# Performance work log

Measured on AMD Instinct MI355X. Metric: run time of the kernel, lower is better.

## Reference

```python
import jax, jax.numpy as jnp
import numpy as np

K = 2
NUM_EXPERTS = 8
NOISE_EPS = 1e-2
GATE_EPS = 1e-6
LOG_EPS = float(np.finfo(np.float64).eps)


def _cv_squared(x):
    # torch .var() is unbiased (ddof=1)
    x = x.astype(jnp.float32)
    return jnp.var(x, ddof=1) / (jnp.mean(x) ** 2 + 1e-10)


def _normal_cdf(x):
    return 0.5 * (1.0 + jax.lax.erf(x * np.float32(1.0 / np.sqrt(2.0))))


def _noisy_top_k_gating(x, noise, w_gate, w_noise):
    B = x.shape[0]
    clean_logits = x @ w_gate                                   # [B, E]
    noise_stddev = jax.nn.softplus(x @ w_noise) + NOISE_EPS     # [B, E]
    noisy_logits = clean_logits + noise * noise_stddev
    probs = jax.nn.softmax(noisy_logits, axis=1)                # softmax before top-k (as in source)
    m = min(K + 1, NUM_EXPERTS)
    top_p, top_idx = jax.lax.top_k(probs, m)                    # [B, m]
    top_k_p = top_p[:, :K]
    top_k_idx = top_idx[:, :K]
    top_k_gates = top_k_p / (jnp.sum(top_k_p, axis=1, keepdims=True) + GATE_EPS)
    gates = jnp.zeros_like(probs).at[jnp.arange(B)[:, None], top_k_idx].set(top_k_gates)
    # load via prob-in-top-k (noisy branch, k < num_experts)
    thr_in = top_p[:, K][:, None]        # (k+1)-th top value
    thr_out = top_p[:, K - 1][:, None]   # k-th top value
    is_in = noisy_logits > thr_in
    prob_if_in = _normal_cdf((clean_logits - thr_in) / noise_stddev)
    prob_if_out = _normal_cdf((clean_logits - thr_out) / noise_stddev)
    load = jnp.sum(jnp.where(is_in, prob_if_in, prob_if_out), axis=0)  # [E]
    return gates, load


def _expert_combine(feat, W, gates):
    # feat [B, D], W [E, D, C], gates [B, E]; expert = linear head + log_softmax
    log_p = jax.nn.log_softmax(jnp.einsum('bd,edc->bec', feat, W), axis=-1)  # [B, E, C]
    # combine: exp(log-scores) * gate, scatter-add over batch, clamp zeros, log
    combined = jnp.einsum('be,bec->bc', gates, jnp.exp(log_p))
    combined = jnp.where(combined == 0, LOG_EPS, combined)
    return jnp.log(combined)


def _moe_forward(sf, of, ppf, pvf, noise, w_gate, w_noise, Ws, Wo, Wp):
    gates, load = _noisy_top_k_gating(sf, noise, w_gate, w_noise)
    importance = jnp.sum(gates, axis=0)
    loss = (_cv_squared(importance) + _cv_squared(load)) * 1e-2
    pf = jnp.concatenate([ppf, pvf], axis=1)  # predicate head input
    ys = _expert_combine(sf, Ws, gates)
    yo = _expert_combine(of, Wo, gates)
    yp = _expert_combine(pf, Wp, gates)
    return ys, yo, yp, loss


def setup_inputs() -> dict:
    key = jax.random.key(0)
    ks = jax.random.split(key, 10)
    B, D, DP, E, C = 4096, 1024, 512, NUM_EXPERTS, 256
    inv = np.float32(1.0 / np.sqrt(D))
    return {
        'sf': jax.random.normal(ks[0], (B, D), jnp.float32),
        'of': jax.random.normal(ks[1], (B, D), jnp.float32),
        'ppf': jax.random.normal(ks[2], (B, DP), jnp.float32),
        'pvf': jax.random.normal(ks[3], (B, DP), jnp.float32),
        'noise': jax.random.normal(ks[4], (B, E), jnp.float32),
        'w_gate': jax.random.normal(ks[5], (D, E), jnp.float32) * 0.02,
        'w_noise': jax.random.normal(ks[6], (D, E), jnp.float32) * 0.02,
        'Ws': jax.random.normal(ks[7], (E, D, C), jnp.float32) * inv,
        'Wo': jax.random.normal(ks[8], (E, D, C), jnp.float32) * inv,
        'Wp': jax.random.normal(ks[9], (E, 2 * DP, C), jnp.float32) * inv,
    }


def reference(sf, of, ppf, pvf, noise, w_gate, w_noise, Ws, Wo, Wp):
    return _moe_forward(sf, of, ppf, pvf, noise, w_gate, w_noise, Ws, Wo, Wp)
```

## Files before the change

### kernel.cpp

```cpp
#include <hip/hip_runtime.h>
#include <math.h>

#define NB 4096
#define DD 1024
#define CC 256
#define NE 8
#define NGBLK 1024

typedef short bf16x8 __attribute__((ext_vector_type(8)));
typedef float f32x4 __attribute__((ext_vector_type(4)));

#define WT_OFF   262144ull
#define PART_OFF 13631488ull
#define PART_ROWS 8224
#define WS_FAST_NEED (41943040ull)

__device__ __forceinline__ unsigned short f2bf(float f) {
    union { float f; unsigned u; } v; v.f = f;
    unsigned x = v.u;
    return (unsigned short)((x + 0x7FFFu + ((x >> 16) & 1u)) >> 16);
}

__global__ __launch_bounds__(256) void gating_kernel(
    const float* __restrict__ sf, const float* __restrict__ noise,
    const float* __restrict__ wg, const float* __restrict__ wn,
    float* __restrict__ gval, int* __restrict__ eidx,
    float* __restrict__ cnt_p, float* __restrict__ imp_p, float* __restrict__ load_p)
{
    int t = threadIdx.x;
    int lane = t & 63;
    int w = t >> 6;
    int b = blockIdx.x * 4 + w;
    const float* x = sf + (size_t)b * DD;

    float accg[8], accn[8];
#pragma unroll
    for (int e = 0; e < 8; e++) { accg[e] = 0.f; accn[e] = 0.f; }

#pragma unroll
    for (int q = 0; q < 16; q++) {
        int d = q * 64 + lane;
        float xs = x[d];
        float4 g0 = *(const float4*)(wg + (size_t)d * 8);
        float4 g1 = *(const float4*)(wg + (size_t)d * 8 + 4);
        float4 n0 = *(const float4*)(wn + (size_t)d * 8);
        float4 n1 = *(const float4*)(wn + (size_t)d * 8 + 4);
        accg[0] += xs * g0.x; accg[1] += xs * g0.y; accg[2] += xs * g0.z; accg[3] += xs * g0.w;
        accg[4] += xs * g1.x; accg[5] += xs * g1.y; accg[6] += xs * g1.z; accg[7] += xs * g1.w;
        accn[0] += xs * n0.x; accn[1] += xs * n0.y; accn[2] += xs * n0.z; accn[3] += xs * n0.w;
        accn[4] += xs * n1.x; accn[5] += xs * n1.y; accn[6] += xs * n1.z; accn[7] += xs * n1.w;
    }
#pragma unroll
    for (int e = 0; e < 8; e++) {
        for (int s = 1; s < 64; s <<= 1) {
            accg[e] += __shfl_xor(accg[e], s);
            accn[e] += __shfl_xor(accn[e], s);
        }
    }

    __shared__ float s_load[4][8], s_imp[4][8], s_cnt[4][8];

    if (lane == 0) {
        float clean[8], stdv[8], noisy[8], p[8];
        float mx = -1e30f;
#pragma unroll
        for (int e = 0; e < 8; e++) {
            clean[e] = accg[e];
            float xn = accn[e];
            float sp = (xn > 0.f) ? (xn + log1pf(expf(-xn))) : log1pf(expf(xn));
            stdv[e] = sp + 0.01f;
            noisy[e] = clean[e] + noise[(size_t)b * 8 + e] * stdv[e];
            mx = fmaxf(mx, noisy[e]);
        }
        float se = 0.f;
#pragma unroll
        for (int e = 0; e < 8; e++) { p[e] = expf(noisy[e] - mx); se += p[e]; }
        float inv = 1.f / se;
#pragma unroll
        for (int e = 0; e < 8; e++) p[e] *= inv;

        int i0 = -1, i1 = -1;
        float p0 = -1e30f, p1v = -1e30f, p2v = -1e30f;
#pragma unroll
        for (int e = 0; e < 8; e++) if (p[e] > p0) { p0 = p[e]; i0 = e; }
#pragma unroll
        for (int e = 0; e < 8; e++) if (e != i0 && p[e] > p1v) { p1v = p[e]; i1 = e; }
#pragma unroll
        for (int e = 0; e < 8; e++) if (e != i0 && e != i1 && p[e] > p2v) { p2v = p[e]; }

        float den = p0 + p1v + 1e-6f;
        float g0 = p0 / den, g1 = p1v / den;
        eidx[2 * b] = i0; eidx[2 * b + 1] = i1;
        gval[2 * b] = g0; gval[2 * b + 1] = g1;

        const float is2 = 0.70710678118654752440f;
#pragma unroll
        for (int e = 0; e < 8; e++) {
            float pin  = 0.5f * (1.f + erff((clean[e] - p2v) / stdv[e] * is2));
            float pout = 0.5f * (1.f + erff((clean[e] - p1v) / stdv[e] * is2));
            s_load[w][e] = (noisy[e] > p2v) ? pin : pout;
            s_imp[w][e]  = (e == i0) ? g0 : (e == i1) ? g1 : 0.f;
            s_cnt[w][e]  = (e == i0 || e == i1) ? 1.f : 0.f;
        }
    }
    __syncthreads();
    if (t < 8) {
        float sl = 0.f, si = 0.f, sc = 0.f;
#pragma unroll
        for (int ww = 0; ww < 4; ww++) {
            sl += s_load[ww][t]; si += s_imp[ww][t]; sc += s_cnt[ww][t];
        }
        load_p[blockIdx.x * 8 + t] = sl;
        imp_p [blockIdx.x * 8 + t] = si;
        cnt_p [blockIdx.x * 8 + t] = sc;
    }
}

__global__ void scan_loss_kernel(const float* __restrict__ cnt_p, const float* __restrict__ imp_p,
                                 const float* __restrict__ load_p,
                                 int* __restrict__ counts, int* __restrict__ off,
                                 int* __restrict__ toff32, int* __restrict__ toff64,
                                 float* __restrict__ out_loss)
{
    __shared__ float s_c[64], s_i[64], s_l[64];
    __shared__ float f_c[8], f_i[8], f_l[8];
    int t = threadIdx.x;
    int e = t & 7, g = t >> 3;
    float sc = 0.f, si = 0.f, sl = 0.f;
    for (int blk = g * 128; blk < (g + 1) * 128; blk++) {
        sc += cnt_p[blk * 8 + e];
        si += imp_p[blk * 8 + e];
        sl += load_p[blk * 8 + e];
    }
    s_c[t] = sc; s_i[t] = si; s_l[t] = sl;
    __syncthreads();
    if (t < 8) {
        float c = 0.f, i = 0.f, l = 0.f;
        for (int gg = 0; gg < 8; gg++) { c += s_c[gg * 8 + t]; i += s_i[gg * 8 + t]; l += s_l[gg * 8 + t]; }
        f_c[t] = c; f_i[t] = i; f_l[t] = l;
        counts[t] = (int)(c + 0.5f);
    }
    __syncthreads();
    if (t == 0) {
        int o = 0, t32 = 0, t64 = 0;
        off[0] = 0; toff32[0] = 0; toff64[0] = 0;
        for (int ee = 0; ee < 8; ee++) {
            int c = (int)(f_c[ee] + 0.5f);
            o += c; off[ee + 1] = o;
            t32 += (c + 31) / 32; toff32[ee + 1] = t32;
            t64 += (c + 63) / 64; toff64[ee + 1] = t64;
        }
        float mi = 0.f, ml = 0.f;
        for (int ee = 0; ee < 8; ee++) { mi += f_i[ee]; ml += f_l[ee]; }
        mi *= 0.125f; ml *= 0.125f;
        float vi = 0.f, vl = 0.f;
        for (int ee = 0; ee < 8; ee++) {
            float di = f_i[ee] - mi; vi += di * di;
            float dl = f_l[ee] - ml; vl += dl * dl;
        }
        vi /= 7.f; vl /= 7.f;
        out_loss[0] = (vi / (mi * mi + 1e-10f) + vl / (ml * ml + 1e-10f)) * 0.01f;
    }
}

__global__ __launch_bounds__(256) void fill_kernel(
    const int* __restrict__ eidx, const int* __restrict__ off, int* __restrict__ rowlist)
{
    __shared__ int hist[256][8];
    __shared__ int off_s[8];
    int t = threadIdx.x;
    if (t < 8) off_s[t] = off[t];
    int base = t * 32;
    int le[32];
    int c[8];
#pragma unroll
    for (int e = 0; e < 8; e++) c[e] = 0;
#pragma unroll
    for (int j = 0; j < 32; j++) {
        int ev = eidx[base + j];
        le[j] = ev;
#pragma unroll
        for (int e = 0; e < 8; e++) c[e] += (ev == e) ? 1 : 0;
    }
#pragma unroll
    for (int e = 0; e < 8; e++) hist[t][e] = c[e];
    __syncthreads();
    if (t < 8) {
        int run = 0;
        for (int i = 0; i < 256; i++) { int v = hist[i][t]; hist[i][t] = run; run += v; }
    }
    __syncthreads();
#pragma unroll
    for (int j = 0; j < 32; j++) {
        int ev = le[j];
        int p = hist[t][ev];
        hist[t][ev] = p + 1;
        rowlist[off_s[ev] + p] = base + j;
    }
}

__global__ __launch_bounds__(256) void prep_w_kernel(
    const float* __restrict__ Ws, const float* __restrict__ Wo, const float* __restrict__ Wp,
    unsigned short* __restrict__ Wt)
{
    __shared__ unsigned short LT[64][68];
    int bid = blockIdx.x;
    int ep = bid >> 6;
    int rem = bid & 63;
    int k0 = (rem >> 2) * 64;
    int c0 = (rem & 3) * 64;
    int strm = ep >> 3, e = ep & 7;
    const float* W = ((strm == 0) ? Ws : (strm == 1) ? Wo : Wp) + (size_t)e * (1024 * 256);

    int t = threadIdx.x;
    int c_l = t & 63;
    int kb = t >> 6;
#pragma unroll
    for (int r = 0; r < 16; r++) {
        int k_l = r * 4 + kb;
        LT[c_l][k_l] = f2bf(W[(size_t)(k0 + k_l) * 256 + c0 + c_l]);
    }
    __syncthreads();

    int cw = t >> 2, kq = t & 3;
    unsigned short* dst_row = Wt + (size_t)ep * 262144 + (size_t)(c0 + cw) * 1024 + k0;
#pragma unroll
    for (int p = 0; p < 2; p++) {
        int kqp = kq + p * 4;
        ushort4 a = *(ushort4*)&LT[cw][kqp * 8];
        ushort4 b = *(ushort4*)&LT[cw][kqp * 8 + 4];
        uint4 o;
        o.x = (unsigned)a.x | ((unsigned)a.y << 16);
        o.y = (unsigned)a.z | ((unsigned)a.w << 16);
        o.z = (unsigned)b.x | ((unsigned)b.y << 16);
        o.w = (unsigned)b.z | ((unsigned)b.w << 16);
        *(uint4*)(dst_row + kqp * 8) = o;
    }
}

__global__ __launch_bounds__(512) void combine_mfma_kernel(
    const float* __restrict__ sf, const float* __restrict__ of,
    const float* __restrict__ ppf, const float* __restrict__ pvf,
    const unsigned short* __restrict__ Wt,
    const int* __restrict__ counts, const int* __restrict__ off, const int* __restrict__ toff64,
    const int* __restrict__ rowlist, const float* __restrict__ gval,
    float* __restrict__ partial)
{
    int bid = blockIdx.x;
    int strm = blockIdx.z;
    if (bid >= toff64[8]) return;
    int e = 0;
    while (bid >= toff64[e + 1]) e++;
    int tm = bid - toff64[e];
    int cnt = counts[e];
    int obase = off[e];
    int ep = strm * 8 + e;

    __shared__ unsigned short A_lds[2][64 * 64];
    __shared__ unsigned short B_lds[2][256 * 64];

    int t = threadIdx.x;
    int l = t & 63, w = t >> 6;
    int wr = w >> 2, wc = w & 3;

    int sm = t >> 3;
    int ss = t & 7;
    int m_st = tm * 64 + sm;
    int pid_st = (m_st < cnt) ? rowlist[obase + m_st] : 8192;
    int arow = (pid_st >= 8192) ? 0 : (pid_st >> 1);
    const float* a01 = (strm == 0) ? (sf + (size_t)arow * DD) : (of + (size_t)arow * DD);
    const float* app = ppf + (size_t)arow * 512;
    const float* apv = pvf + (size_t)arow * 512;
    const unsigned short* bsrc = Wt + (size_t)ep * 262144 + (size_t)sm * 1024 + ss * 8;
    int aw = sm * 64 + ((ss ^ (sm & 7)) * 8);
    int bw = (ss ^ (sm & 7)) * 8;

#define LOAD_A(ko, dst)                                                    \
    {                                                                      \
        int kk = (ko) + ss * 8;                                            \
        const float* s_;                                                   \
        if (strm != 2) s_ = a01 + kk;                                      \
        else s_ = (kk < 512) ? (app + kk) : (apv + (kk - 512));            \
        float4 f0 = *(const float4*)s_;                                    \
        float4 f1 = *(const float4*)(s_ + 4);                              \
        dst.x = (unsigned)f2bf(f0.x) | ((unsigned)f2bf(f0.y) << 16);       \
        dst.y = (unsigned)f2bf(f0.z) | ((unsigned)f2bf(f0.w) << 16);       \
        dst.z = (unsigned)f2bf(f1.x) | ((unsigned)f2bf(f1.y) << 16);       \
        dst.w = (unsigned)f2bf(f1.z) | ((unsigned)f2bf(f1.w) << 16);       \
    }

    {
        uint4 ra; LOAD_A(0, ra);
        uint4 rb[4];
#pragma unroll
        for (int q = 0; q < 4; q++) rb[q] = *(const uint4*)(bsrc + q * 65536);
        *(uint4*)&A_lds[0][aw] = ra;
#pragma unroll
        for (int q = 0; q < 4; q++) *(uint4*)&B_lds[0][(sm + q * 64) * 64 + bw] = rb[q];
    }

    f32x4 acc[2][4];
#pragma unroll
    for (int i = 0; i < 2; i++)
#pragma unroll
        for (int j = 0; j < 4; j++)
#pragma unroll
            for (int r = 0; r < 4; r++) acc[i][j][r] = 0.f;

    int g = l >> 4;
    int axor = l & 7;

    for (int kt = 0; kt < 16; kt++) {
        int cur = kt & 1;
        uint4 ra; uint4 rb[4];
        if (kt < 15) {
            int ko = (kt + 1) * 64;
            LOAD_A(ko, ra);
#pragma unroll
            for (int q = 0; q < 4; q++) rb[q] = *(const uint4*)(bsrc + q * 65536 + ko);
        }
        __syncthreads();
#pragma unroll
        for (int kw = 0; kw < 2; kw++) {
            int slot = ((kw * 4 + g) ^ axor) * 8;
            bf16x8 af[2], bf[4];
#pragma unroll
            for (int i = 0; i < 2; i++)
                af[i] = *(const bf16x8*)&A_lds[cur][(wr * 32 + (l & 15) + i * 16) * 64 + slot];
#pragma unroll
            for (int j = 0; j < 4; j++)
                bf[j] = *(const bf16x8*)&B_lds[cur][(wc * 64 + j * 16 + (l & 15)) * 64 + slot];
#pragma unroll
            for (int i = 0; i < 2; i++)
#pragma unroll
                for (int j = 0; j < 4; j++)
                    acc[i][j] = __builtin_amdgcn_mfma_f32_16x16x32_bf16(af[i], bf[j], acc[i][j], 0, 0, 0);
        }
        if (kt < 15) {
            *(uint4*)&A_lds[cur ^ 1][aw] = ra;
#pragma unroll
            for (int q = 0; q < 4; q++) *(uint4*)&B_lds[cur ^ 1][(sm + q * 64) * 64 + bw] = rb[q];
        }
    }
#undef LOAD_A

    __syncthreads();
    float* s_red = (float*)&A_lds[0][0];

    float gate_r[2][4];
    int pid_r[2][4];
#pragma unroll
    for (int i = 0; i < 2; i++)
#pragma unroll
        for (int r = 0; r < 4; r++) {
            int row = wr * 32 + i * 16 + g * 4 + r;
            int m = tm * 64 + row;
            int pid = (m < cnt) ? rowlist[obase + m] : 8192;
            pid_r[i][r] = pid;
            gate_r[i][r] = (m < cnt) ? gval[pid] : 0.f;
        }

    float rmx[2][4], scale[2][4];
#pragma unroll
    for (int i = 0; i < 2; i++)
#pragma unroll
        for (int r = 0; r < 4; r++) {
            float mx = -1e30f;
#pragma unroll
            for (int j = 0; j < 4; j++) mx = fmaxf(mx, acc[i][j][r]);
#pragma unroll
            for (int s = 1; s < 16; s <<= 1) mx = fmaxf(mx, __shfl_xor(mx, s));
            if ((l & 15) == 0) s_red[(wr * 32 + i * 16 + g * 4 + r) * 4 + wc] = mx;
        }
    __syncthreads();
#pragma unroll
    for (int i = 0; i < 2; i++)
#pragma unroll
        for (int r = 0; r < 4; r++) {
            int row = wr * 32 + i * 16 + g * 4 + r;
            rmx[i][r] = fmaxf(fmaxf(s_red[row * 4 + 0], s_red[row * 4 + 1]),
                              fmaxf(s_red[row * 4 + 2], s_red[row * 4 + 3]));
        }
    __syncthreads();
#pragma unroll
    for (int i = 0; i < 2; i++)
#pragma unroll
        for (int r = 0; r < 4; r++) {
            float se = 0.f;
#pragma unroll
            for (int j = 0; j < 4; j++) {
                float v = __expf(acc[i][j][r] - rmx[i][r]);
                acc[i][j][r] = v;
                se += v;
            }
#pragma unroll
            for (int s = 1; s < 16; s <<= 1) se += __shfl_xor(se, s);
            if ((l & 15) == 0) s_red[(wr * 32 + i * 16 + g * 4 + r) * 4 + wc] = se;
        }
    __syncthreads();
#pragma unroll
    for (int i = 0; i < 2; i++)
#pragma unroll
        for (int r = 0; r < 4; r++) {
            int row = wr * 32 + i * 16 + g * 4 + r;
            float tot = s_red[row * 4 + 0] + s_red[row * 4 + 1] + s_red[row * 4 + 2] + s_red[row * 4 + 3];
            scale[i][r] = gate_r[i][r] / tot;
        }

    float* pbase = partial + (size_t)strm * (PART_ROWS * 256);
#pragma unroll
    for (int i = 0; i < 2; i++)
#pragma unroll
        for (int r = 0; r < 4; r++) {
            float* pr = pbase + (size_t)pid_r[i][r] * 256;
            float sc = scale[i][r];
#pragma unroll
            for (int j = 0; j < 4; j++) {
                int col = wc * 64 + j * 16 + (l & 15);
                pr[col] = acc[i][j][r] * sc;
            }
        }
}

__global__ void log_pair_kernel(const float* __restrict__ partial, float* __restrict__ out, int n4)
{
    int i = blockIdx.x * 256 + threadIdx.x;
    if (i >= n4) return;
    int flat = i * 4;
    int strm = flat >> 20;
    int rem = flat & 1048575;
    int b = rem >> 8;
    int c = rem & 255;
    const float* p0 = partial + (size_t)strm * (PART_ROWS * 256) + (size_t)(2 * b) * 256 + c;
    float4 v0 = *(const float4*)p0;
    float4 v1 = *(const float4*)(p0 + 256);
    const float EPSL = 2.2204460492503131e-16f;
    float4 v;
    v.x = v0.x + v1.x; v.y = v0.y + v1.y; v.z = v0.z + v1.z; v.w = v0.w + v1.w;
    v.x = logf(v.x == 0.f ? EPSL : v.x);
    v.y = logf(v.y == 0.f ? EPSL : v.y);
    v.z = logf(v.z == 0.f ? EPSL : v.z);
    v.w = logf(v.w == 0.f ? EPSL : v.w);
    *(float4*)(out + (size_t)flat) = v;
}

__global__ __launch_bounds__(256) void combine_kernel(
    const float* __restrict__ sf, const float* __restrict__ of,
    const float* __restrict__ ppf, const float* __restrict__ pvf,
    const float* __restrict__ Ws, const float* __restrict__ Wo, const float* __restrict__ Wp,
    const int* __restrict__ counts, const int* __restrict__ off, const int* __restrict__ toff,
    const int* __restrict__ rowlist, const float* __restrict__ gval,
    float* __restrict__ out)
{
    int bid = blockIdx.x;
    int strm = blockIdx.z;
    if (bid >= toff[8]) return;
    int e = 0;
    while (bid >= toff[e + 1]) e++;
    int tm = bid - toff[e];
    int cnt = counts[e];
    int obase = off[e];

    __shared__ float As[32][36];
    __shared__ float Bs[32][256];
    __shared__ int rows_s[32];
    __shared__ float gate_s[32];

    int t = threadIdx.x;
    if (t < 32) {
        int m = tm * 32 + t;
        if (m < cnt) {
            int pid = rowlist[obase + m];
            rows_s[t] = pid >> 1;
            gate_s[t] = gval[pid];
        } else {
            rows_s[t] = -1;
            gate_s[t] = 0.f;
        }
    }
    __syncthreads();

    const float* W = ((strm == 0) ? Ws : (strm == 1) ? Wo : Wp) + (size_t)e * DD * CC;
    float acc[2][16];
#pragma unroll
    for (int i = 0; i < 2; i++)
#pragma unroll
        for (int j = 0; j < 16; j++) acc[i][j] = 0.f;

    int tx = t & 15, ty = t >> 4;
    int r_st = t >> 3, d4 = t & 7;
    int row_st = rows_s[r_st];

    for (int k0 = 0; k0 < DD; k0 += 32) {
        float4 v = make_float4(0.f, 0.f, 0.f, 0.f);
        if (row_st >= 0) {
            int d = k0 + d4 * 4;
            if (strm == 0)      v = *(const float4*)(sf + (size_t)row_st * DD + d);
            else if (strm == 1) v = *(const float4*)(of + (size_t)row_st * DD + d);
            else v = (d < 512) ? *(const float4*)(ppf + (size_t)row_st * 512 + d)
                               : *(const float4*)(pvf + (size_t)row_st * 512 + (d - 512));
        }
        As[d4 * 4 + 0][r_st] = v.x;
        As[d4 * 4 + 1][r_st] = v.y;
        As[d4 * 4 + 2][r_st] = v.z;
        As[d4 * 4 + 3][r_st] = v.w;
#pragma unroll
        for (int j = 0; j < 8; j++) {
            int vv = t + 256 * j;
            int k = vv >> 6, c4 = vv & 63;
            *(float4*)&Bs[k][c4 * 4] = *(const float4*)&W[(size_t)(k0 + k) * CC + c4 * 4];
        }
        __syncthreads();

#pragma unroll
        for (int k = 0; k < 32; k++) {
            float2 a = *(float2*)&As[k][ty * 2];
#pragma unroll
            for (int jj = 0; jj < 4; jj++) {
                float4 bb = *(float4*)&Bs[k][jj * 64 + tx * 4];
                acc[0][jj * 4 + 0] += a.x * bb.x;
                acc[0][jj * 4 + 1] += a.x * bb.y;
                acc[0][jj * 4 + 2] += a.x * bb.z;
                acc[0][jj * 4 + 3] += a.x * bb.w;
                acc[1][jj * 4 + 0] += a.y * bb.x;
                acc[1][jj * 4 + 1] += a.y * bb.y;
                acc[1][jj * 4 + 2] += a.y * bb.z;
                acc[1][jj * 4 + 3] += a.y * bb.w;
            }
        }
        __syncthreads();
    }

    float* comb = out + (size_t)strm * (NB * CC);
#pragma unroll
    for (int i = 0; i < 2; i++) {
        int r = ty * 2 + i;
        int row = rows_s[r];
        if (row < 0) continue;
        float mx = -1e30f;
#pragma unroll
        for (int j = 0; j < 16; j++) mx = fmaxf(mx, acc[i][j]);
        for (int s = 1; s < 16; s <<= 1) mx = fmaxf(mx, __shfl_xor(mx, s, 16));
        float se = 0.f;
#pragma unroll
        for (int j = 0; j < 16; j++) { acc[i][j] = expf(acc[i][j] - mx); se += acc[i][j]; }
        for (int s = 1; s < 16; s <<= 1) se += __shfl_xor(se, s, 16);
        float scale = gate_s[r] / se;
#pragma unroll
        for (int jj = 0; jj < 4; jj++)
#pragma unroll
            for (int jo = 0; jo < 4; jo++) {
                int col = jj * 64 + tx * 4 + jo;
                atomicAdd(comb + (size_t)row * CC + col, acc[i][jj * 4 + jo] * scale);
            }
    }
}

__global__ void log_kernel(float* __restrict__ out, int n4)
{
    int i = blockIdx.x * 256 + threadIdx.x;
    if (i >= n4) return;
    float4 v = *(float4*)(out + (size_t)i * 4);
    const float EPSL = 2.2204460492503131e-16f;
    v.x = logf(v.x == 0.f ? EPSL : v.x);
    v.y = logf(v.y == 0.f ? EPSL : v.y);
    v.z = logf(v.z == 0.f ? EPSL : v.z);
    v.w = logf(v.w == 0.f ? EPSL : v.w);
    *(float4*)(out + (size_t)i * 4) = v;
}

extern "C" void kernel_launch(void* const* d_in, const int* in_sizes, int n_in,
                              void* d_out, int out_size, void* d_ws, size_t ws_size,
                              hipStream_t stream) {
    (void)in_sizes; (void)n_in;
    const float* sf    = (const float*)d_in[0];
    const float* of    = (const float*)d_in[1];
    const float* ppf   = (const float*)d_in[2];
    const float* pvf   = (const float*)d_in[3];
    const float* noise = (const float*)d_in[4];
    const float* wg    = (const float*)d_in[5];
    const float* wn    = (const float*)d_in[6];
    const float* Ws    = (const float*)d_in[7];
    const float* Wo    = (const float*)d_in[8];
    const float* Wp    = (const float*)d_in[9];
    float* out = (float*)d_out;

    char* ws = (char*)d_ws;
    int*   off     = (int*)(ws + 64);
    int*   toff32  = (int*)(ws + 104);
    int*   counts  = (int*)(ws + 144);
    int*   toff64  = (int*)(ws + 184);
    float* gval    = (float*)(ws + 256);
    int*   eidx    = (int*)(ws + 33024);
    int*   rowlist = (int*)(ws + 65792);
    float* cnt_p   = (float*)(ws + 98560);
    float* imp_p   = (float*)(ws + 131328);
    float* load_p  = (float*)(ws + 164096);
    unsigned short* Wt = (unsigned short*)(ws + WT_OFF);
    float* partial = (float*)(ws + PART_OFF);

    bool fast = ws_size >= WS_FAST_NEED;

    if (fast) {
        prep_w_kernel<<<1536, 256, 0, stream>>>(Ws, Wo, Wp, Wt);
    } else {
        hipMemsetAsync(d_out, 0, (size_t)out_size * sizeof(float), stream);
    }

    gating_kernel<<<NGBLK, 256, 0, stream>>>(sf, noise, wg, wn, gval, eidx, cnt_p, imp_p, load_p);
    scan_loss_kernel<<<1, 64, 0, stream>>>(cnt_p, imp_p, load_p, counts, off, toff32, toff64, out + (out_size - 1));
    fill_kernel<<<1, 256, 0, stream>>>(eidx, off, rowlist);

    int n4 = (out_size - 1) / 4;
    if (fast) {
        combine_mfma_kernel<<<dim3(136, 1, 3), 512, 0, stream>>>(
            sf, of, ppf, pvf, Wt, counts, off, toff64, rowlist, gval, partial);
        log_pair_kernel<<<(n4 + 255) / 256, 256, 0, stream>>>(partial, out, n4);
    } else {
        combine_kernel<<<dim3(2 * NB / 32 + 8, 1, 3), 256, 0, stream>>>(
            sf, of, ppf, pvf, Ws, Wo, Wp, counts, off, toff32, rowlist, gval, out);
        log_kernel<<<(n4 + 255) / 256, 256, 0, stream>>>(out, n4);
    }
}
```

Baseline: 260.9 us.

## Shrink MoE combine tile to 32 rows, stage gating weights in LDS, fuse scan and fill

The combine MFMA kernel moves from 64-row tiles with 8 waves and K-step 64 to 32-row tiles with 4 waves and K-step 32. This doubles the grid to spread work across more CUs and uses a new rotated LDS swizzle. The gating kernel now stages w_gate and w_noise in LDS and processes 16 rows per block with vectorised x loads. The scan/loss and fill kernels are merged into one launch. The trade-off is that each weight tile is now reused across fewer rows, so B-matrix reload traffic per row doubles.

```diff
diff --git a/kernel.cpp b/kernel.cpp
--- a/kernel.cpp
+++ b/kernel.cpp
@@ -5,7 +5,7 @@
 #define DD 1024
 #define CC 256
 #define NE 8
-#define NGBLK 1024
+#define NGBLK_G 256
 
 typedef short bf16x8 __attribute__((ext_vector_type(8)));
 typedef float f32x4 __attribute__((ext_vector_type(4)));
@@ -27,80 +27,102 @@
     float* __restrict__ gval, int* __restrict__ eidx,
     float* __restrict__ cnt_p, float* __restrict__ imp_p, float* __restrict__ load_p)
 {
+    __shared__ float wgs[8][1024];
+    __shared__ float wns[8][1024];
+    __shared__ float s_load[4][8], s_imp[4][8], s_cnt[4][8];
+
     int t = threadIdx.x;
     int lane = t & 63;
     int w = t >> 6;
-    int b = blockIdx.x * 4 + w;
-    const float* x = sf + (size_t)b * DD;
-
-    float accg[8], accn[8];
-#pragma unroll
-    for (int e = 0; e < 8; e++) { accg[e] = 0.f; accn[e] = 0.f; }
-
-#pragma unroll
-    for (int q = 0; q < 16; q++) {
-        int d = q * 64 + lane;
-        float xs = x[d];
-        float4 g0 = *(const float4*)(wg + (size_t)d * 8);
-        float4 g1 = *(const float4*)(wg + (size_t)d * 8 + 4);
-        float4 n0 = *(const float4*)(wn + (size_t)d * 8);
-        float4 n1 = *(const float4*)(wn + (size_t)d * 8 + 4);
-        accg[0] += xs * g0.x; accg[1] += xs * g0.y; accg[2] += xs * g0.z; accg[3] += xs * g0.w;
-        accg[4] += xs * g1.x; accg[5] += xs * g1.y; accg[6] += xs * g1.z; accg[7] += xs * g1.w;
-        accn[0] += xs * n0.x; accn[1] += xs * n0.y; accn[2] += xs * n0.z; accn[3] += xs * n0.w;
-        accn[4] += xs * n1.x; accn[5] += xs * n1.y; accn[6] += xs * n1.z; accn[7] += xs * n1.w;
-    }
-#pragma unroll
-    for (int e = 0; e < 8; e++) {
-        for (int s = 1; s < 64; s <<= 1) {
-            accg[e] += __shfl_xor(accg[e], s);
-            accn[e] += __shfl_xor(accn[e], s);
-        }
-    }
-
-    __shared__ float s_load[4][8], s_imp[4][8], s_cnt[4][8];
-
+
+    for (int i = 0; i < 32; i++) {
+        int f = i * 256 + t;
+        int d = f >> 3, e = f & 7;
+        wgs[e][d] = wg[f];
+        wns[e][d] = wn[f];
+    }
+    __syncthreads();
+
+    float lload[8], limp[8], lcnt[8];
+#pragma unroll
+    for (int e = 0; e < 8; e++) { lload[e] = 0.f; limp[e] = 0.f; lcnt[e] = 0.f; }
+
+    for (int rr = 0; rr < 4; rr++) {
+        int b = blockIdx.x * 16 + w * 4 + rr;
+        const float* x = sf + (size_t)b * DD;
+
+        float accg[8], accn[8];
+#pragma unroll
+        for (int e = 0; e < 8; e++) { accg[e] = 0.f; accn[e] = 0.f; }
+
+#pragma unroll
+        for (int q = 0; q < 4; q++) {
+            int d0 = q * 256 + lane * 4;
+            float4 xv = *(const float4*)(x + d0);
+#pragma unroll
+            for (int e = 0; e < 8; e++) {
+                float4 g4 = *(const float4*)&wgs[e][d0];
+                float4 n4 = *(const float4*)&wns[e][d0];
+                accg[e] += xv.x * g4.x + xv.y * g4.y + xv.z * g4.z + xv.w * g4.w;
+                accn[e] += xv.x * n4.x + xv.y * n4.y + xv.z * n4.z + xv.w * n4.w;
+            }
+        }
+#pragma unroll
+        for (int e = 0; e < 8; e++) {
+            for (int s = 1; s < 64; s <<= 1) {
+                accg[e] += __shfl_xor(accg[e], s);
+                accn[e] += __shfl_xor(accn[e], s);
+            }
+        }
+
+        if (lane == 0) {
+            float clean[8], stdv[8], noisy[8], p[8];
+            float mx = -1e30f;
+#pragma unroll
+            for (int e = 0; e < 8; e++) {
+                clean[e] = accg[e];
+                float xn = accn[e];
+                float sp = (xn > 0.f) ? (xn + log1pf(expf(-xn))) : log1pf(expf(xn));
+                stdv[e] = sp + 0.01f;
+                noisy[e] = clean[e] + noise[(size_t)b * 8 + e] * stdv[e];
+                mx = fmaxf(mx, noisy[e]);
+            }
+            float se = 0.f;
+#pragma unroll
+            for (int e = 0; e < 8; e++) { p[e] = expf(noisy[e] - mx); se += p[e]; }
+            float inv = 1.f / se;
+#pragma unroll
+            for (int e = 0; e < 8; e++) p[e] *= inv;
+
+            int i0 = -1, i1 = -1;
+            float p0 = -1e30f, p1v = -1e30f, p2v = -1e30f;
+#pragma unroll
+            for (int e = 0; e < 8; e++) if (p[e] > p0) { p0 = p[e]; i0 = e; }
+#pragma unroll
+            for (int e = 0; e < 8; e++) if (e != i0 && p[e] > p1v) { p1v = p[e]; i1 = e; }
+#pragma unroll
+            for (int e = 0; e < 8; e++) if (e != i0 && e != i1 && p[e] > p2v) { p2v = p[e]; }
+
+            float den = p0 + p1v + 1e-6f;
+            float g0 = p0 / den, g1 = p1v / den;
+            eidx[2 * b] = i0; eidx[2 * b + 1] = i1;
+            gval[2 * b] = g0; gval[2 * b + 1] = g1;
+
+            const float is2 = 0.70710678118654752440f;
+#pragma unroll
+            for (int e = 0; e < 8; e++) {
+                float pin  = 0.5f * (1.f + erff((clean[e] - p2v) / stdv[e] * is2));
+                float pout = 0.5f * (1.f + erff((clean[e] - p1v) / stdv[e] * is2));
+                lload[e] += (noisy[e] > p2v) ? pin : pout;
+                limp[e]  += (e == i0) ? g0 : (e == i1) ? g1 : 0.f;
+                lcnt[e]  += (e == i0 || e == i1) ? 1.f : 0.f;
+            }
+        }
+    }
     if (lane == 0) {
-        float clean[8], stdv[8], noisy[8], p[8];
-        float mx = -1e30f;
 #pragma unroll
         for (int e = 0; e < 8; e++) {
-            clean[e] = accg[e];
-            float xn = accn[e];
-            float sp = (xn > 0.f) ? (xn + log1pf(expf(-xn))) : log1pf(expf(xn));
-            stdv[e] = sp + 0.01f;
-            noisy[e] = clean[e] + noise[(size_t)b * 8 + e] * stdv[e];
-            mx = fmaxf(mx, noisy[e]);
-        }
-        float se = 0.f;
-#pragma unroll
-        for (int e = 0; e < 8; e++) { p[e] = expf(noisy[e] - mx); se += p[e]; }
-        float inv = 1.f / se;
-#pragma unroll
-        for (int e = 0; e < 8; e++) p[e] *= inv;
-
-        int i0 = -1, i1 = -1;
-        float p0 = -1e30f, p1v = -1e30f, p2v = -1e30f;
-#pragma unroll
-        for (int e = 0; e < 8; e++) if (p[e] > p0) { p0 = p[e]; i0 = e; }
-#pragma unroll
-        for (int e = 0; e < 8; e++) if (e != i0 && p[e] > p1v) { p1v = p[e]; i1 = e; }
-#pragma unroll
-        for (int e = 0; e < 8; e++) if (e != i0 && e != i1 && p[e] > p2v) { p2v = p[e]; }
-
-        float den = p0 + p1v + 1e-6f;
-        float g0 = p0 / den, g1 = p1v / den;
-        eidx[2 * b] = i0; eidx[2 * b + 1] = i1;
-        gval[2 * b] = g0; gval[2 * b + 1] = g1;
-
-        const float is2 = 0.70710678118654752440f;
-#pragma unroll
-        for (int e = 0; e < 8; e++) {
-            float pin  = 0.5f * (1.f + erff((clean[e] - p2v) / stdv[e] * is2));
-            float pout = 0.5f * (1.f + erff((clean[e] - p1v) / stdv[e] * is2));
-            s_load[w][e] = (noisy[e] > p2v) ? pin : pout;
-            s_imp[w][e]  = (e == i0) ? g0 : (e == i1) ? g1 : 0.f;
-            s_cnt[w][e]  = (e == i0 || e == i1) ? 1.f : 0.f;
+            s_load[w][e] = lload[e]; s_imp[w][e] = limp[e]; s_cnt[w][e] = lcnt[e];
         }
     }
     __syncthreads();
@@ -116,18 +138,22 @@
     }
 }
 
-__global__ void scan_loss_kernel(const float* __restrict__ cnt_p, const float* __restrict__ imp_p,
-                                 const float* __restrict__ load_p,
-                                 int* __restrict__ counts, int* __restrict__ off,
-                                 int* __restrict__ toff32, int* __restrict__ toff64,
-                                 float* __restrict__ out_loss)
+__global__ __launch_bounds__(256) void scan_fill_kernel(
+    const float* __restrict__ cnt_p, const float* __restrict__ imp_p,
+    const float* __restrict__ load_p, const int* __restrict__ eidx,
+    int* __restrict__ counts, int* __restrict__ off,
+    int* __restrict__ toff32, int* __restrict__ toff64,
+    int* __restrict__ rowlist, float* __restrict__ out_loss)
 {
-    __shared__ float s_c[64], s_i[64], s_l[64];
+    __shared__ float s_c[256], s_i[256], s_l[256];
     __shared__ float f_c[8], f_i[8], f_l[8];
+    __shared__ int off_s[8];
+    __shared__ int hist[256][8];
+
     int t = threadIdx.x;
     int e = t & 7, g = t >> 3;
     float sc = 0.f, si = 0.f, sl = 0.f;
-    for (int blk = g * 128; blk < (g + 1) * 128; blk++) {
+    for (int blk = g * 8; blk < g * 8 + 8; blk++) {
         sc += cnt_p[blk * 8 + e];
         si += imp_p[blk * 8 + e];
         sl += load_p[blk * 8 + e];
@@ -136,7 +162,7 @@
     __syncthreads();
     if (t < 8) {
         float c = 0.f, i = 0.f, l = 0.f;
-        for (int gg = 0; gg < 8; gg++) { c += s_c[gg * 8 + t]; i += s_i[gg * 8 + t]; l += s_l[gg * 8 + t]; }
+        for (int gg = 0; gg < 32; gg++) { c += s_c[gg * 8 + t]; i += s_i[gg * 8 + t]; l += s_l[gg * 8 + t]; }
         f_c[t] = c; f_i[t] = i; f_l[t] = l;
         counts[t] = (int)(c + 0.5f);
     }
@@ -146,6 +172,7 @@
         off[0] = 0; toff32[0] = 0; toff64[0] = 0;
         for (int ee = 0; ee < 8; ee++) {
             int c = (int)(f_c[ee] + 0.5f);
+            off_s[ee] = o;
             o += c; off[ee + 1] = o;
             t32 += (c + 31) / 32; toff32[ee + 1] = t32;
             t64 += (c + 63) / 64; toff64[ee + 1] = t64;
@@ -161,29 +188,22 @@
         vi /= 7.f; vl /= 7.f;
         out_loss[0] = (vi / (mi * mi + 1e-10f) + vl / (ml * ml + 1e-10f)) * 0.01f;
     }
-}
-
-__global__ __launch_bounds__(256) void fill_kernel(
-    const int* __restrict__ eidx, const int* __restrict__ off, int* __restrict__ rowlist)
-{
-    __shared__ int hist[256][8];
-    __shared__ int off_s[8];
-    int t = threadIdx.x;
-    if (t < 8) off_s[t] = off[t];
+    __syncthreads();
+
     int base = t * 32;
     int le[32];
-    int c[8];
-#pragma unroll
-    for (int e = 0; e < 8; e++) c[e] = 0;
+    int c8[8];
+#pragma unroll
+    for (int ee = 0; ee < 8; ee++) c8[ee] = 0;
 #pragma unroll
     for (int j = 0; j < 32; j++) {
         int ev = eidx[base + j];
         le[j] = ev;
 #pragma unroll
-        for (int e = 0; e < 8; e++) c[e] += (ev == e) ? 1 : 0;
-    }
-#pragma unroll
-    for (int e = 0; e < 8; e++) hist[t][e] = c[e];
+        for (int ee = 0; ee < 8; ee++) c8[ee] += (ev == ee) ? 1 : 0;
+    }
+#pragma unroll
+    for (int ee = 0; ee < 8; ee++) hist[t][ee] = c8[ee];
     __syncthreads();
     if (t < 8) {
         int run = 0;
@@ -238,46 +258,54 @@
     }
 }
 
-__global__ __launch_bounds__(512) void combine_mfma_kernel(
+__global__ __launch_bounds__(256) void combine_mfma_kernel(
     const float* __restrict__ sf, const float* __restrict__ of,
     const float* __restrict__ ppf, const float* __restrict__ pvf,
     const unsigned short* __restrict__ Wt,
-    const int* __restrict__ counts, const int* __restrict__ off, const int* __restrict__ toff64,
+    const int* __restrict__ counts, const int* __restrict__ off, const int* __restrict__ toff32,
     const int* __restrict__ rowlist, const float* __restrict__ gval,
     float* __restrict__ partial)
 {
     int bid = blockIdx.x;
     int strm = blockIdx.z;
-    if (bid >= toff64[8]) return;
+    if (bid >= toff32[8]) return;
     int e = 0;
-    while (bid >= toff64[e + 1]) e++;
-    int tm = bid - toff64[e];
+    while (bid >= toff32[e + 1]) e++;
+    int tm = bid - toff32[e];
     int cnt = counts[e];
     int obase = off[e];
     int ep = strm * 8 + e;
 
-    __shared__ unsigned short A_lds[2][64 * 64];
-    __shared__ unsigned short B_lds[2][256 * 64];
+    __shared__ unsigned short A_lds[2][32 * 32];
+    __shared__ unsigned short B_lds[2][256 * 32];
 
     int t = threadIdx.x;
     int l = t & 63, w = t >> 6;
-    int wr = w >> 2, wc = w & 3;
-
-    int sm = t >> 3;
-    int ss = t & 7;
-    int m_st = tm * 64 + sm;
-    int pid_st = (m_st < cnt) ? rowlist[obase + m_st] : 8192;
+
+    int sb_row0 = t >> 2;
+    int sb_s = t & 3;
+    const unsigned short* bsrc = Wt + (size_t)ep * 262144 + (size_t)sb_row0 * 1024 + sb_s * 8;
+    int bw_off[4];
+#pragma unroll
+    for (int jj = 0; jj < 4; jj++) {
+        int row = sb_row0 + 64 * jj;
+        bw_off[jj] = row * 32 + (((sb_s + (row >> 1)) & 3) * 8);
+    }
+
+    bool a_act = (t < 128);
+    int sa_row = t >> 2;
+    int sa_s = t & 3;
+    int m_st = tm * 32 + sa_row;
+    int pid_st = (a_act && m_st < cnt) ? rowlist[obase + m_st] : 8192;
     int arow = (pid_st >= 8192) ? 0 : (pid_st >> 1);
     const float* a01 = (strm == 0) ? (sf + (size_t)arow * DD) : (of + (size_t)arow * DD);
     const float* app = ppf + (size_t)arow * 512;
     const float* apv = pvf + (size_t)arow * 512;
-    const unsigned short* bsrc = Wt + (size_t)ep * 262144 + (size_t)sm * 1024 + ss * 8;
-    int aw = sm * 64 + ((ss ^ (sm & 7)) * 8);
-    int bw = (ss ^ (sm & 7)) * 8;
-
-#define LOAD_A(ko, dst)                                                    \
+    int aw_off = sa_row * 32 + (((sa_s + (sa_row >> 1)) & 3) * 8);
+
+#define LOAD_A(kt, dst)                                                    \
     {                                                                      \
-        int kk = (ko) + ss * 8;                                            \
+        int kk = (kt) * 32 + sa_s * 8;                                     \
         const float* s_;                                                   \
         if (strm != 2) s_ = a01 + kk;                                      \
         else s_ = (kk < 512) ? (app + kk) : (apv + (kk - 512));            \
@@ -290,13 +318,13 @@
     }
 
     {
-        uint4 ra; LOAD_A(0, ra);
         uint4 rb[4];
 #pragma unroll
-        for (int q = 0; q < 4; q++) rb[q] = *(const uint4*)(bsrc + q * 65536);
-        *(uint4*)&A_lds[0][aw] = ra;
-#pragma unroll
-        for (int q = 0; q < 4; q++) *(uint4*)&B_lds[0][(sm + q * 64) * 64 + bw] = rb[q];
+        for (int jj = 0; jj < 4; jj++) rb[jj] = *(const uint4*)(bsrc + (size_t)jj * 65536);
+        uint4 ra;
+        if (a_act) { LOAD_A(0, ra); *(uint4*)&A_lds[0][aw_off] = ra; }
+#pragma unroll
+        for (int jj = 0; jj < 4; jj++) *(uint4*)&B_lds[0][bw_off[jj]] = rb[jj];
     }
 
     f32x4 acc[2][4];
@@ -308,38 +336,43 @@
             for (int r = 0; r < 4; r++) acc[i][j][r] = 0.f;
 
     int g = l >> 4;
-    int axor = l & 7;
-
-    for (int kt = 0; kt < 16; kt++) {
+    int c15 = l & 15;
+
+    int af_off[2], bf_off[4];
+#pragma unroll
+    for (int i = 0; i < 2; i++) {
+        int row = i * 16 + c15;
+        af_off[i] = row * 32 + (((g + (row >> 1)) & 3) * 8);
+    }
+#pragma unroll
+    for (int j = 0; j < 4; j++) {
+        int c = w * 64 + j * 16 + c15;
+        bf_off[j] = c * 32 + (((g + (c >> 1)) & 3) * 8);
+    }
+
+    for (int kt = 0; kt < 32; kt++) {
         int cur = kt & 1;
         uint4 ra; uint4 rb[4];
-        if (kt < 15) {
-            int ko = (kt + 1) * 64;
-            LOAD_A(ko, ra);
-#pragma unroll
-            for (int q = 0; q < 4; q++) rb[q] = *(const uint4*)(bsrc + q * 65536 + ko);
+        if (kt < 31) {
+#pragma unroll
+            for (int jj = 0; jj < 4; jj++) rb[jj] = *(const uint4*)(bsrc + (size_t)jj * 65536 + (kt + 1) * 32);
+            if (a_act) LOAD_A(kt + 1, ra);
         }
         __syncthreads();
-#pragma unroll
-        for (int kw = 0; kw < 2; kw++) {
-            int slot = ((kw * 4 + g) ^ axor) * 8;
-            bf16x8 af[2], bf[4];
-#pragma unroll
-            for (int i = 0; i < 2; i++)
-                af[i] = *(const bf16x8*)&A_lds[cur][(wr * 32 + (l & 15) + i * 16) * 64 + slot];
+        bf16x8 af[2], bf[4];
+#pragma unroll
+        for (int i = 0; i < 2; i++) af[i] = *(const bf16x8*)&A_lds[cur][af_off[i]];
+#pragma unroll
+        for (int j = 0; j < 4; j++) bf[j] = *(const bf16x8*)&B_lds[cur][bf_off[j]];
+#pragma unroll
+        for (int i = 0; i < 2; i++)
 #pragma unroll
             for (int j = 0; j < 4; j++)
-                bf[j] = *(const bf16x8*)&B_lds[cur][(wc * 64 + j * 16 + (l & 15)) * 64 + slot];
-#pragma unroll
-            for (int i = 0; i < 2; i++)
-#pragma unroll
-                for (int j = 0; j < 4; j++)
-                    acc[i][j] = __builtin_amdgcn_mfma_f32_16x16x32_bf16(af[i], bf[j], acc[i][j], 0, 0, 0);
-        }
-        if (kt < 15) {
-            *(uint4*)&A_lds[cur ^ 1][aw] = ra;
-#pragma unroll
-            for (int q = 0; q < 4; q++) *(uint4*)&B_lds[cur ^ 1][(sm + q * 64) * 64 + bw] = rb[q];
+                acc[i][j] = __builtin_amdgcn_mfma_f32_16x16x32_bf16(af[i], bf[j], acc[i][j], 0, 0, 0);
+        if (kt < 31) {
+            if (a_act) *(uint4*)&A_lds[cur ^ 1][aw_off] = ra;
+#pragma unroll
+            for (int jj = 0; jj < 4; jj++) *(uint4*)&B_lds[cur ^ 1][bw_off[jj]] = rb[jj];
         }
     }
 #undef LOAD_A
@@ -353,8 +386,8 @@
     for (int i = 0; i < 2; i++)
 #pragma unroll
         for (int r = 0; r < 4; r++) {
-            int row = wr * 32 + i * 16 + g * 4 + r;
-            int m = tm * 64 + row;
+            int row = i * 16 + g * 4 + r;
+            int m = tm * 32 + row;
             int pid = (m < cnt) ? rowlist[obase + m] : 8192;
             pid_r[i][r] = pid;
             gate_r[i][r] = (m < cnt) ? gval[pid] : 0.f;
@@ -370,14 +403,14 @@
             for (int j = 0; j < 4; j++) mx = fmaxf(mx, acc[i][j][r]);
 #pragma unroll
             for (int s = 1; s < 16; s <<= 1) mx = fmaxf(mx, __shfl_xor(mx, s));
-            if ((l & 15) == 0) s_red[(wr * 32 + i * 16 + g * 4 + r) * 4 + wc] = mx;
+            if (c15 == 0) s_red[(i * 16 + g * 4 + r) * 4 + w] = mx;
         }
     __syncthreads();
 #pragma unroll
     for (int i = 0; i < 2; i++)
 #pragma unroll
         for (int r = 0; r < 4; r++) {
-            int row = wr * 32 + i * 16 + g * 4 + r;
+            int row = i * 16 + g * 4 + r;
             rmx[i][r] = fmaxf(fmaxf(s_red[row * 4 + 0], s_red[row * 4 + 1]),
                               fmaxf(s_red[row * 4 + 2], s_red[row * 4 + 3]));
         }
@@ -395,14 +428,14 @@
             }
 #pragma unroll
             for (int s = 1; s < 16; s <<= 1) se += __shfl_xor(se, s);
-            if ((l & 15) == 0) s_red[(wr * 32 + i * 16 + g * 4 + r) * 4 + wc] = se;
+            if (c15 == 0) s_red[(i * 16 + g * 4 + r) * 4 + w] = se;
         }
     __syncthreads();
 #pragma unroll
     for (int i = 0; i < 2; i++)
 #pragma unroll
         for (int r = 0; r < 4; r++) {
-            int row = wr * 32 + i * 16 + g * 4 + r;
+            int row = i * 16 + g * 4 + r;
             float tot = s_red[row * 4 + 0] + s_red[row * 4 + 1] + s_red[row * 4 + 2] + s_red[row * 4 + 3];
             scale[i][r] = gate_r[i][r] / tot;
         }
@@ -416,7 +449,7 @@
             float sc = scale[i][r];
 #pragma unroll
             for (int j = 0; j < 4; j++) {
-                int col = wc * 64 + j * 16 + (l & 15);
+                int col = w * 64 + j * 16 + c15;
                 pr[col] = acc[i][j][r] * sc;
             }
         }
@@ -607,17 +640,17 @@
         hipMemsetAsync(d_out, 0, (size_t)out_size * sizeof(float), stream);
     }
 
-    gating_kernel<<<NGBLK, 256, 0, stream>>>(sf, noise, wg, wn, gval, eidx, cnt_p, imp_p, load_p);
-    scan_loss_kernel<<<1, 64, 0, stream>>>(cnt_p, imp_p, load_p, counts, off, toff32, toff64, out + (out_size - 1));
-    fill_kernel<<<1, 256, 0, stream>>>(eidx, off, rowlist);
+    gating_kernel<<<NGBLK_G, 256, 0, stream>>>(sf, noise, wg, wn, gval, eidx, cnt_p, imp_p, load_p);
+    scan_fill_kernel<<<1, 256, 0, stream>>>(cnt_p, imp_p, load_p, eidx,
+                                            counts, off, toff32, toff64, rowlist, out + (out_size - 1));
 
     int n4 = (out_size - 1) / 4;
     if (fast) {
-        combine_mfma_kernel<<<dim3(136, 1, 3), 512, 0, stream>>>(
-            sf, of, ppf, pvf, Wt, counts, off, toff64, rowlist, gval, partial);
+        combine_mfma_kernel<<<dim3(264, 1, 3), 256, 0, stream>>>(
+            sf, of, ppf, pvf, Wt, counts, off, toff32, rowlist, gval, partial);
         log_pair_kernel<<<(n4 + 255) / 256, 256, 0, stream>>>(partial, out, n4);
     } else {
-        combine_kernel<<<dim3(2 * NB / 32 + 8, 1, 3), 256, 0, stream>>>(
+        combine_kernel<<<dim3(264, 1, 3), 256, 0, stream>>>(
             sf, of, ppf, pvf, Ws, Wo, Wp, counts, off, toff32, rowlist, gval, out);
         log_kernel<<<(n4 + 255) / 256, 256, 0, stream>>>(out, n4);
     }
```

After: 350.8 us. 34.5% more time.
